# Kernel tuning notes

Measured on AMD Instinct MI355X. Metric: run time of the kernel, lower is better.

The kernel has to match this reference:

```python
import jax, jax.numpy as jnp
from jax import lax
import numpy as np

WIN = 15
PAD = WIN // 2  # floor(15/2) = 7


def _box_sum(x):
    """Sum over a 15x15 window, stride 1, zero padding 7 (same as F.conv2d
    with an all-ones [1,1,15,15] filter). Done separably (H then W) for
    efficiency; math is identical to the dense ones-filter conv."""
    kh = jnp.ones((1, 1, WIN, 1), x.dtype)
    kw = jnp.ones((1, 1, 1, WIN), x.dtype)
    x = lax.conv_general_dilated(x, kh, (1, 1), [(PAD, PAD), (0, 0)])
    x = lax.conv_general_dilated(x, kw, (1, 1), [(0, 0), (PAD, PAD)])
    return x


def setup_inputs() -> dict:
    key = jax.random.key(0)
    k1, k2 = jax.random.split(key)
    B, C, H, W = 16, 1, 512, 512
    I = jax.random.uniform(k1, (B, C, H, W), dtype=jnp.float32)
    J = jax.random.uniform(k2, (B, C, H, W), dtype=jnp.float32)
    return {"I": I, "J": J}


def reference(I, J):
    win_size = jnp.asarray(WIN * WIN, I.dtype)

    I_sum = _box_sum(I)
    J_sum = _box_sum(J)
    I2_sum = _box_sum(I * I)
    J2_sum = _box_sum(J * J)
    IJ_sum = _box_sum(I * J)

    u_I = I_sum / win_size
    u_J = J_sum / win_size

    cross = IJ_sum - u_J * I_sum - u_I * J_sum + u_I * u_J * win_size
    I_var = I2_sum - 2 * u_I * I_sum + u_I * u_I * win_size
    J_var = J2_sum - 2 * u_J * J_sum + u_J * u_J * win_size

    # NOTE: faithful to the torch code — cc is a GLOBAL scalar ratio,
    # so torch.mean(cc) == cc.
    cc = jnp.sum(cross) / jnp.sqrt(jnp.sum(I_var) * jnp.sum(J_var))
    return -cc
```

## Files before the change

kernel.cpp:

```cpp
#include <hip/hip_runtime.h>
#include <math.h>


#define IMG_H 512
#define IMG_W 512
#define NB    16
#define TILE  32
#define HALO  7
#define SPAN  46
#define LSTR  47
#define VSTR  49
#define NTX   16
#define NTY   16
#define NBLK  (NB * NTX * NTY)

__device__ __forceinline__ float winw(int i) {
    int a = i < 7 ? i : 7;
    int b = (511 - i) < 7 ? (511 - i) : 7;
    return (float)(a + b + 1);
}

__global__ __launch_bounds__(256) void ncc_main(const float* __restrict__ I,
                                                const float* __restrict__ J,
                                                float* __restrict__ partials) {
    __shared__ float lI[SPAN * LSTR];
    __shared__ float lJ[SPAN * LSTR];
    __shared__ float vI[TILE * VSTR];
    __shared__ float vJ[TILE * VSTR];
    __shared__ float red[4 * 6];

    const int tid = threadIdx.x;
    const int tx = blockIdx.x, ty = blockIdx.y, bz = blockIdx.z;
    const int R0 = ty * TILE - HALO;
    const int C0 = tx * TILE - HALO;
    const float* Ib = I + (size_t)bz * IMG_H * IMG_W;
    const float* Jb = J + (size_t)bz * IMG_H * IMG_W;

    for (int k = tid; k < SPAN * SPAN; k += 256) {
        int r = k / SPAN;
        int c = k - r * SPAN;
        int gr = R0 + r, gc = C0 + c;
        float iv = 0.0f, jv = 0.0f;
        if (gr >= 0 && gr < IMG_H && gc >= 0 && gc < IMG_W) {
            int gidx = gr * IMG_W + gc;
            iv = Ib[gidx];
            jv = Jb[gidx];
        }
        lI[r * LSTR + c] = iv;
        lJ[r * LSTR + c] = jv;
    }
    __syncthreads();

    {
        int c = tid % SPAN;
        int chunk = tid / SPAN;
        if (chunk < 4) {
            int r0 = chunk * 8;
            float sI = 0.0f, sJ = 0.0f;
            #pragma unroll
            for (int dr = 0; dr < 15; ++dr) {
                sI += lI[(r0 + dr) * LSTR + c];
                sJ += lJ[(r0 + dr) * LSTR + c];
            }
            vI[r0 * VSTR + c] = sI;
            vJ[r0 * VSTR + c] = sJ;
            #pragma unroll
            for (int r = 1; r < 8; ++r) {
                int rr = r0 + r;
                sI += lI[(rr + 14) * LSTR + c] - lI[(rr - 1) * LSTR + c];
                sJ += lJ[(rr + 14) * LSTR + c] - lJ[(rr - 1) * LSTR + c];
                vI[rr * VSTR + c] = sI;
                vJ[rr * VSTR + c] = sJ;
            }
        }
    }
    __syncthreads();

    float acc0 = 0.f, acc1 = 0.f, acc2 = 0.f, acc3 = 0.f, acc4 = 0.f, acc5 = 0.f;
    {
        int r = tid & 31;
        int chunk = tid >> 5;
        int c0 = chunk * 4;
        float sI = 0.0f, sJ = 0.0f;
        #pragma unroll
        for (int dc = 0; dc < 15; ++dc) {
            sI += vI[r * VSTR + c0 + dc];
            sJ += vJ[r * VSTR + c0 + dc];
        }
        float chw = winw(ty * TILE + r);
        #pragma unroll
        for (int i = 0; i < 4; ++i) {
            int c = c0 + i;
            if (i > 0) {
                sI += vI[r * VSTR + c + 14] - vI[r * VSTR + c - 1];
                sJ += vJ[r * VSTR + c + 14] - vJ[r * VSTR + c - 1];
            }
            acc3 += sI * sJ;
            acc4 += sI * sI;
            acc5 += sJ * sJ;
            float iv = lI[(r + HALO) * LSTR + c + HALO];
            float jv = lJ[(r + HALO) * LSTR + c + HALO];
            float w = chw * winw(tx * TILE + c);
            acc0 += iv * jv * w;
            acc1 += iv * iv * w;
            acc2 += jv * jv * w;
        }
    }

    float vals[6] = {acc0, acc1, acc2, acc3, acc4, acc5};
    #pragma unroll
    for (int k = 0; k < 6; ++k) {
        float v = vals[k];
        #pragma unroll
        for (int off = 32; off > 0; off >>= 1) v += __shfl_down(v, off, 64);
        vals[k] = v;
    }
    int wave = tid >> 6, lane = tid & 63;
    if (lane == 0) {
        #pragma unroll
        for (int k = 0; k < 6; ++k) red[wave * 6 + k] = vals[k];
    }
    __syncthreads();
    if (tid == 0) {
        int bidx = (bz * NTY + ty) * NTX + tx;
        #pragma unroll
        for (int k = 0; k < 6; ++k) {
            partials[bidx * 6 + k] = red[k] + red[6 + k] + red[12 + k] + red[18 + k];
        }
    }
}

__global__ __launch_bounds__(256) void ncc_finalize(const float* __restrict__ partials,
                                                    float* __restrict__ out) {
    __shared__ double red[4 * 6];
    int tid = threadIdx.x;
    double acc[6] = {0, 0, 0, 0, 0, 0};
    for (int b = tid; b < NBLK; b += 256) {
        #pragma unroll
        for (int k = 0; k < 6; ++k) acc[k] += (double)partials[b * 6 + k];
    }
    #pragma unroll
    for (int k = 0; k < 6; ++k) {
        double v = acc[k];
        #pragma unroll
        for (int off = 32; off > 0; off >>= 1) v += __shfl_down(v, off, 64);
        acc[k] = v;
    }
    int wave = tid >> 6, lane = tid & 63;
    if (lane == 0) {
        #pragma unroll
        for (int k = 0; k < 6; ++k) red[wave * 6 + k] = acc[k];
    }
    __syncthreads();
    if (tid == 0) {
        double s[6];
        #pragma unroll
        for (int k = 0; k < 6; ++k) s[k] = red[k] + red[6 + k] + red[12 + k] + red[18 + k];
        double A = s[0], Bv = s[1], Cv = s[2], D = s[3], E = s[4], F = s[5];
        double num = A - D / 225.0;
        double varI = Bv - E / 225.0;
        double varJ = Cv - F / 225.0;
        double cc = num / sqrt(varI * varJ);
        out[0] = (float)(-cc);
    }
}

extern "C" void kernel_launch(void* const* d_in, const int* in_sizes, int n_in,
                              void* d_out, int out_size, void* d_ws, size_t ws_size,
                              hipStream_t stream) {
    const float* I = (const float*)d_in[0];
    const float* J = (const float*)d_in[1];
    float* partials = (float*)d_ws;

    dim3 grid(NTX, NTY, NB);
    ncc_main<<<grid, 256, 0, stream>>>(I, J, partials);
    ncc_finalize<<<1, 256, 0, stream>>>(partials, (float*)d_out);
}
```

Baseline: 101.0 us.

## Widen tiles to 64x32, fuse weighted products into load loop, register-cache row sums

Tiles grow from 32x32 to 64x32, which cuts the halo overhead per output pixel and halves the block count. The weighted I*J, I*I and J*J sums now accumulate during the global load loop, so the interior pixels are no longer reread from shared memory. Each thread handles 8 columns and loads its 22 vertical-sum values into registers before the horizontal sliding sum. The costs are more registers and LDS per block and a vertical pass where only 234 of 256 threads work, with uneven row counts per chunk.

Result: no change. 99.64 us (-1.4%).

```diff
diff --git a/kernel.cpp b/kernel.cpp
--- a/kernel.cpp
+++ b/kernel.cpp
@@ -5,12 +5,14 @@
 #define IMG_H 512
 #define IMG_W 512
 #define NB    16
-#define TILE  32
+#define TW    64
+#define TH    32
 #define HALO  7
-#define SPAN  46
-#define LSTR  47
-#define VSTR  49
-#define NTX   16
+#define SPAN_R 46
+#define SPAN_C 78
+#define LSTR  78
+#define VSTR  79
+#define NTX   8
 #define NTY   16
 #define NBLK  (NB * NTX * NTY)
 
@@ -23,91 +25,95 @@
 __global__ __launch_bounds__(256) void ncc_main(const float* __restrict__ I,
                                                 const float* __restrict__ J,
                                                 float* __restrict__ partials) {
-    __shared__ float lI[SPAN * LSTR];
-    __shared__ float lJ[SPAN * LSTR];
-    __shared__ float vI[TILE * VSTR];
-    __shared__ float vJ[TILE * VSTR];
+    __shared__ float lI[SPAN_R * LSTR];
+    __shared__ float lJ[SPAN_R * LSTR];
+    __shared__ float vI[TH * VSTR];
+    __shared__ float vJ[TH * VSTR];
     __shared__ float red[4 * 6];
 
     const int tid = threadIdx.x;
     const int tx = blockIdx.x, ty = blockIdx.y, bz = blockIdx.z;
-    const int R0 = ty * TILE - HALO;
-    const int C0 = tx * TILE - HALO;
+    const int R0 = ty * TH - HALO;
+    const int C0 = tx * TW - HALO;
     const float* Ib = I + (size_t)bz * IMG_H * IMG_W;
     const float* Jb = J + (size_t)bz * IMG_H * IMG_W;
 
-    for (int k = tid; k < SPAN * SPAN; k += 256) {
-        int r = k / SPAN;
-        int c = k - r * SPAN;
+    float a0 = 0.f, a1 = 0.f, a2 = 0.f;
+
+    for (int k = tid; k < SPAN_R * SPAN_C; k += 256) {
+        int r = k / SPAN_C;
+        int c = k - r * SPAN_C;
         int gr = R0 + r, gc = C0 + c;
         float iv = 0.0f, jv = 0.0f;
-        if (gr >= 0 && gr < IMG_H && gc >= 0 && gc < IMG_W) {
+        if ((unsigned)gr < (unsigned)IMG_H && (unsigned)gc < (unsigned)IMG_W) {
             int gidx = gr * IMG_W + gc;
             iv = Ib[gidx];
             jv = Jb[gidx];
         }
         lI[r * LSTR + c] = iv;
         lJ[r * LSTR + c] = jv;
+        if (r >= HALO && r < HALO + TH && c >= HALO && c < HALO + TW) {
+            float w = winw(gr) * winw(gc);
+            a0 += iv * jv * w;
+            a1 += iv * iv * w;
+            a2 += jv * jv * w;
+        }
     }
     __syncthreads();
 
     {
-        int c = tid % SPAN;
-        int chunk = tid / SPAN;
-        if (chunk < 4) {
-            int r0 = chunk * 8;
+        int cid = tid % SPAN_C;
+        int chunk = tid / SPAN_C;
+        if (chunk < 3) {
+            int r0 = chunk * 11;
+            int nr = (chunk == 2) ? 10 : 11;
             float sI = 0.0f, sJ = 0.0f;
             #pragma unroll
             for (int dr = 0; dr < 15; ++dr) {
-                sI += lI[(r0 + dr) * LSTR + c];
-                sJ += lJ[(r0 + dr) * LSTR + c];
+                sI += lI[(r0 + dr) * LSTR + cid];
+                sJ += lJ[(r0 + dr) * LSTR + cid];
             }
-            vI[r0 * VSTR + c] = sI;
-            vJ[r0 * VSTR + c] = sJ;
-            #pragma unroll
-            for (int r = 1; r < 8; ++r) {
-                int rr = r0 + r;
-                sI += lI[(rr + 14) * LSTR + c] - lI[(rr - 1) * LSTR + c];
-                sJ += lJ[(rr + 14) * LSTR + c] - lJ[(rr - 1) * LSTR + c];
-                vI[rr * VSTR + c] = sI;
-                vJ[rr * VSTR + c] = sJ;
+            vI[r0 * VSTR + cid] = sI;
+            vJ[r0 * VSTR + cid] = sJ;
+            for (int r = r0 + 1; r < r0 + nr; ++r) {
+                sI += lI[(r + 14) * LSTR + cid] - lI[(r - 1) * LSTR + cid];
+                sJ += lJ[(r + 14) * LSTR + cid] - lJ[(r - 1) * LSTR + cid];
+                vI[r * VSTR + cid] = sI;
+                vJ[r * VSTR + cid] = sJ;
             }
         }
     }
     __syncthreads();
 
-    float acc0 = 0.f, acc1 = 0.f, acc2 = 0.f, acc3 = 0.f, acc4 = 0.f, acc5 = 0.f;
+    float a3 = 0.f, a4 = 0.f, a5 = 0.f;
     {
         int r = tid & 31;
-        int chunk = tid >> 5;
-        int c0 = chunk * 4;
+        int ch = tid >> 5;
+        int c0 = ch * 8;
+        int base = r * VSTR + c0;
+        float va[22], vb[22];
+        #pragma unroll
+        for (int i = 0; i < 22; ++i) {
+            va[i] = vI[base + i];
+            vb[i] = vJ[base + i];
+        }
         float sI = 0.0f, sJ = 0.0f;
         #pragma unroll
-        for (int dc = 0; dc < 15; ++dc) {
-            sI += vI[r * VSTR + c0 + dc];
-            sJ += vJ[r * VSTR + c0 + dc];
-        }
-        float chw = winw(ty * TILE + r);
+        for (int i = 0; i < 15; ++i) { sI += va[i]; sJ += vb[i]; }
+        a3 += sI * sJ;
+        a4 += sI * sI;
+        a5 += sJ * sJ;
         #pragma unroll
-        for (int i = 0; i < 4; ++i) {
-            int c = c0 + i;
-            if (i > 0) {
-                sI += vI[r * VSTR + c + 14] - vI[r * VSTR + c - 1];
-                sJ += vJ[r * VSTR + c + 14] - vJ[r * VSTR + c - 1];
-            }
-            acc3 += sI * sJ;
-            acc4 += sI * sI;
-            acc5 += sJ * sJ;
-            float iv = lI[(r + HALO) * LSTR + c + HALO];
-            float jv = lJ[(r + HALO) * LSTR + c + HALO];
-            float w = chw * winw(tx * TILE + c);
-            acc0 += iv * jv * w;
-            acc1 += iv * iv * w;
-            acc2 += jv * jv * w;
+        for (int i = 1; i < 8; ++i) {
+            sI += va[i + 14] - va[i - 1];
+            sJ += vb[i + 14] - vb[i - 1];
+            a3 += sI * sJ;
+            a4 += sI * sI;
+            a5 += sJ * sJ;
         }
     }
 
-    float vals[6] = {acc0, acc1, acc2, acc3, acc4, acc5};
+    float vals[6] = {a0, a1, a2, a3, a4, a5};
     #pragma unroll
     for (int k = 0; k < 6; ++k) {
         float v = vals[k];
```
